# Optimization experiments

Measured on AMD Instinct MI355X. Metric: run time of the kernel, lower is better.

The kernel has to match this reference:

```python
import jax, jax.numpy as jnp
import numpy as np

N_NODES = 100000
N_EDGES = 3200000
F_IN = 128
CHANNELS = 128


def setup_inputs() -> dict:
    key = jax.random.key(0)
    k1, k2, k3, k4, k5 = jax.random.split(key, 5)
    x = jax.random.normal(k1, (N_NODES, F_IN), dtype=jnp.float32)
    kernel = jax.random.normal(k2, (F_IN, CHANNELS), dtype=jnp.float32) * (1.0 / np.sqrt(F_IN))
    bias = jnp.zeros((CHANNELS,), dtype=jnp.float32)
    edge_row = jnp.sort(jax.random.randint(k3, (N_EDGES,), 0, N_NODES, dtype=jnp.int32))
    edge_col = jax.random.randint(k4, (N_EDGES,), 0, N_NODES, dtype=jnp.int32)
    edge_val = jax.random.uniform(k5, (N_EDGES,), dtype=jnp.float32)
    return {"x": x, "kernel": kernel, "bias": bias, "edge_val": edge_val,
            "edge_row": edge_row, "edge_col": edge_col}


def reference(x, kernel, bias, edge_val, edge_row, edge_col):
    # Z = relu(A_tilde @ (X @ W) + b), A_tilde given in COO form (row, col, val)
    n = x.shape[0]
    xw = x @ kernel                              # [N, C] dense projection
    msgs = xw[edge_col] * edge_val[:, None]      # [E, C] gather + scale
    agg = jax.ops.segment_sum(msgs, edge_row, num_segments=n)  # SpMM scatter
    return jax.nn.relu(agg + bias)
```

## Files before the change

kernel.cpp:

```cpp
#include <hip/hip_runtime.h>

#define F_IN 128
#define CH   128

typedef __attribute__((ext_vector_type(8))) short bf16x8;
typedef __attribute__((ext_vector_type(4))) float f32x4;
typedef __attribute__((ext_vector_type(4))) unsigned u32x4;

static __device__ __forceinline__ ushort f2b(float f) {
  union { float f; unsigned u; } v; v.f = f;
  const unsigned u = v.u;
  return (ushort)((u + 0x7FFFu + ((u >> 16) & 1u)) >> 16);
}

__global__ __launch_bounds__(512) void gemm_rowptr_fused(
    const float* __restrict__ x, const float* __restrict__ w,
    unsigned char* __restrict__ xwq, float* __restrict__ scale,
    const int* __restrict__ edge_row, int* __restrict__ row_ptr,
    int n, int n_edges, int gemm_blocks) {
  __shared__ __align__(16) ushort Wt[F_IN * CH];
  const int t = threadIdx.x;

  if ((int)blockIdx.x >= gemm_blocks) {
    const int r = ((int)blockIdx.x - gemm_blocks) * 512 + t;
    if (r <= n) {
      int lo = 0, hi = n_edges;
      while (lo < hi) {
        const int mid = (lo + hi) >> 1;
        if (edge_row[mid] < r) lo = mid + 1; else hi = mid;
      }
      row_ptr[r] = lo;
    }
    return;
  }

  for (int i = t; i < (F_IN * CH) / 4; i += 512) {
    const int k  = i >> 5;
    const int n4 = (i & 31) << 2;
    const f32x4 wv = *(const f32x4*)&w[k * CH + n4];
#pragma unroll
    for (int q = 0; q < 4; ++q) {
      const int nn = n4 + q;
      const int byte = (nn * 256 + k * 2) ^ ((nn & 7) << 4);
      *(ushort*)((char*)Wt + byte) = f2b(wv[q]);
    }
  }
  __syncthreads();

  const int wave = t >> 6, lane = t & 63;
  const int R0   = blockIdx.x * 128 + wave * 16;
  const int arow = R0 + (lane & 15);
  const int kgrp = (lane >> 4) * 8;

  bf16x8 a[4];
#pragma unroll
  for (int s = 0; s < 4; ++s) {
    if (arow < n) {
      const f32x4 p0 = __builtin_nontemporal_load(
          (const f32x4*)&x[arow * F_IN + s * 32 + kgrp]);
      const f32x4 p1 = __builtin_nontemporal_load(
          (const f32x4*)&x[arow * F_IN + s * 32 + kgrp + 4]);
#pragma unroll
      for (int j = 0; j < 4; ++j) {
        a[s][j]     = (short)f2b(p0[j]);
        a[s][j + 4] = (short)f2b(p1[j]);
      }
    } else {
#pragma unroll
      for (int j = 0; j < 8; ++j) a[s][j] = (short)0;
    }
  }

  f32x4 acc[8];
#pragma unroll
  for (int t8 = 0; t8 < 8; ++t8) acc[t8] = (f32x4){0.f, 0.f, 0.f, 0.f};

#pragma unroll
  for (int t8 = 0; t8 < 8; ++t8) {
    const int col = t8 * 16 + (lane & 15);
#pragma unroll
    for (int s = 0; s < 4; ++s) {
      const int byte = (col * 256 + (s * 32 + kgrp) * 2) ^ ((col & 7) << 4);
      const bf16x8 b = *(const bf16x8*)((const char*)Wt + byte);
      acc[t8] = __builtin_amdgcn_mfma_f32_16x16x32_bf16(a[s], b, acc[t8], 0, 0, 0);
    }
  }

  const int li = lane & 15;
  const int r0 = R0 + (lane >> 4) * 4;
#pragma unroll
  for (int i = 0; i < 4; ++i) {
    const int rr = r0 + i;
    float m = 0.f;
#pragma unroll
    for (int t8 = 0; t8 < 8; ++t8) m = fmaxf(m, fabsf(acc[t8][i]));
    m = fmaxf(m, __shfl_xor(m, 1));
    m = fmaxf(m, __shfl_xor(m, 2));
    m = fmaxf(m, __shfl_xor(m, 4));
    m = fmaxf(m, __shfl_xor(m, 8));
    const float inv = (m > 1e-20f) ? 127.f / m : 0.f;
    if (rr < n) {
      if (li == 0) scale[rr] = m * (1.f / 127.f);
#pragma unroll
      for (int t8 = 0; t8 < 8; ++t8) {
        const float q = rintf(acc[t8][i] * inv) + 128.f;
        xwq[rr * CH + t8 * 16 + li] = (unsigned char)q;
      }
    }
  }
}

#define ACC16(U, V)                                                     \
  do {                                                                  \
    acc[ 0] = fmaf((V), (float)((U)[0]         & 0xFFu), acc[ 0]);      \
    acc[ 1] = fmaf((V), (float)(((U)[0] >>  8) & 0xFFu), acc[ 1]);      \
    acc[ 2] = fmaf((V), (float)(((U)[0] >> 16) & 0xFFu), acc[ 2]);      \
    acc[ 3] = fmaf((V), (float)((U)[0] >> 24),           acc[ 3]);      \
    acc[ 4] = fmaf((V), (float)((U)[1]         & 0xFFu), acc[ 4]);      \
    acc[ 5] = fmaf((V), (float)(((U)[1] >>  8) & 0xFFu), acc[ 5]);      \
    acc[ 6] = fmaf((V), (float)(((U)[1] >> 16) & 0xFFu), acc[ 6]);      \
    acc[ 7] = fmaf((V), (float)((U)[1] >> 24),           acc[ 7]);      \
    acc[ 8] = fmaf((V), (float)((U)[2]         & 0xFFu), acc[ 8]);      \
    acc[ 9] = fmaf((V), (float)(((U)[2] >>  8) & 0xFFu), acc[ 9]);      \
    acc[10] = fmaf((V), (float)(((U)[2] >> 16) & 0xFFu), acc[10]);      \
    acc[11] = fmaf((V), (float)((U)[2] >> 24),           acc[11]);      \
    acc[12] = fmaf((V), (float)((U)[3]         & 0xFFu), acc[12]);      \
    acc[13] = fmaf((V), (float)(((U)[3] >>  8) & 0xFFu), acc[13]);      \
    acc[14] = fmaf((V), (float)(((U)[3] >> 16) & 0xFFu), acc[14]);      \
    acc[15] = fmaf((V), (float)((U)[3] >> 24),           acc[15]);      \
  } while (0)

__global__ __launch_bounds__(256) void spmm_rowwave(
    const unsigned char* __restrict__ xwq, const float* __restrict__ scale,
    const float* __restrict__ edge_val, const int* __restrict__ edge_col,
    const int* __restrict__ row_ptr, const float* __restrict__ bias,
    float* __restrict__ out, int n) {
  const int wid = (int)((blockIdx.x * blockDim.x + threadIdx.x) >> 6);
  if (wid >= n) return;
  const int lane = threadIdx.x & 63;
  const int g8 = lane >> 3;
  const int l8 = lane & 7;
  const int start = row_ptr[wid], end = row_ptr[wid + 1];
  const u32x4* __restrict__ xw4 = (const u32x4*)xwq;

  float acc[16];
#pragma unroll
  for (int j = 0; j < 16; ++j) acc[j] = 0.f;
  float S = 0.f;

  for (int e0 = start; e0 < end; e0 += 64) {
    const int e = e0 + lane;
    int   c_my = 0;
    float vp_my = 0.f;
    if (e < end) {
      c_my = __builtin_nontemporal_load(edge_col + e);
      const float v = __builtin_nontemporal_load(edge_val + e);
      vp_my = v * scale[c_my];
    }
    S += vp_my;

#pragma unroll
    for (int it = 0; it < 8; ++it) {
      const int src  = it * 8 + g8;
      const int   c  = __shfl(c_my, src);
      const float vp = __shfl(vp_my, src);
      const u32x4 u = xw4[c * 8 + l8];
      ACC16(u, vp);
    }
  }

  S += __shfl_xor(S, 1);
  S += __shfl_xor(S, 2);
  S += __shfl_xor(S, 4);
  S += __shfl_xor(S, 8);
  S += __shfl_xor(S, 16);
  S += __shfl_xor(S, 32);

#pragma unroll
  for (int j = 0; j < 16; ++j) {
    acc[j] += __shfl_xor(acc[j], 8);
    acc[j] += __shfl_xor(acc[j], 16);
    acc[j] += __shfl_xor(acc[j], 32);
  }

  if (g8 == 0) {
    const int c = l8 * 16;
    const float off = 128.f * S;
#pragma unroll
    for (int q = 0; q < 4; ++q) {
      const f32x4 bv = *(const f32x4*)&bias[c + q * 4];
      f32x4 o;
      o[0] = fmaxf(acc[q * 4 + 0] - off + bv[0], 0.f);
      o[1] = fmaxf(acc[q * 4 + 1] - off + bv[1], 0.f);
      o[2] = fmaxf(acc[q * 4 + 2] - off + bv[2], 0.f);
      o[3] = fmaxf(acc[q * 4 + 3] - off + bv[3], 0.f);
      __builtin_nontemporal_store(o, (f32x4*)&out[(size_t)wid * CH + c + q * 4]);
    }
  }
}

extern "C" void kernel_launch(void* const* d_in, const int* in_sizes, int n_in,
                              void* d_out, int out_size, void* d_ws, size_t ws_size,
                              hipStream_t stream) {
  const float* x        = (const float*)d_in[0];
  const float* kernel   = (const float*)d_in[1];
  const float* bias     = (const float*)d_in[2];
  const float* edge_val = (const float*)d_in[3];
  const int*   edge_row = (const int*)d_in[4];
  const int*   edge_col = (const int*)d_in[5];
  float* out = (float*)d_out;

  const int n       = in_sizes[0] / F_IN;
  const int n_edges = in_sizes[3];

  unsigned char* xwq = (unsigned char*)d_ws;
  float* scale = (float*)((char*)d_ws + (size_t)n * CH);
  int* rowptr  = (int*)((char*)d_ws + (size_t)n * CH + (size_t)n * sizeof(float));

  const int GB = (n + 127) / 128;
  const int RB = (n + 1 + 511) / 512;
  gemm_rowptr_fused<<<GB + RB, 512, 0, stream>>>(x, kernel, xwq, scale,
                                                 edge_row, rowptr,
                                                 n, n_edges, GB);

  spmm_rowwave<<<(n + 3) / 4, 256, 0, stream>>>(xwq, scale, edge_val, edge_col,
                                                rowptr, bias, out, n);
}
```

Before: 132.1 us.

## Map sixteen lanes per row in SpMM with LDS-broadcast columns and packed FMA

The SpMM kernel moves from one 64-lane wave per row to sixteen lanes per row, each lane owning 8 output channels. Edge columns and scaled values are staged in shared memory, so each lane issues sixteen independent 8-byte gathers before accumulating with packed two-wide FMAs. This removes the cross-lane accumulator reduction and the idle lanes at the average degree of about 32, and adds memory-level parallelism. It relies on wave-synchronous LDS use without a barrier and uses more registers for the batched gathers.

```diff
diff --git a/kernel.cpp b/kernel.cpp
--- a/kernel.cpp
+++ b/kernel.cpp
@@ -5,7 +5,8 @@
 
 typedef __attribute__((ext_vector_type(8))) short bf16x8;
 typedef __attribute__((ext_vector_type(4))) float f32x4;
-typedef __attribute__((ext_vector_type(4))) unsigned u32x4;
+typedef __attribute__((ext_vector_type(2))) float f32x2;
+typedef __attribute__((ext_vector_type(2))) unsigned u32x2;
 
 static __device__ __forceinline__ ushort f2b(float f) {
   union { float f; unsigned u; } v; v.f = f;
@@ -110,62 +111,74 @@
   }
 }
 
-#define ACC16(U, V)                                                     \
-  do {                                                                  \
-    acc[ 0] = fmaf((V), (float)((U)[0]         & 0xFFu), acc[ 0]);      \
-    acc[ 1] = fmaf((V), (float)(((U)[0] >>  8) & 0xFFu), acc[ 1]);      \
-    acc[ 2] = fmaf((V), (float)(((U)[0] >> 16) & 0xFFu), acc[ 2]);      \
-    acc[ 3] = fmaf((V), (float)((U)[0] >> 24),           acc[ 3]);      \
-    acc[ 4] = fmaf((V), (float)((U)[1]         & 0xFFu), acc[ 4]);      \
-    acc[ 5] = fmaf((V), (float)(((U)[1] >>  8) & 0xFFu), acc[ 5]);      \
-    acc[ 6] = fmaf((V), (float)(((U)[1] >> 16) & 0xFFu), acc[ 6]);      \
-    acc[ 7] = fmaf((V), (float)((U)[1] >> 24),           acc[ 7]);      \
-    acc[ 8] = fmaf((V), (float)((U)[2]         & 0xFFu), acc[ 8]);      \
-    acc[ 9] = fmaf((V), (float)(((U)[2] >>  8) & 0xFFu), acc[ 9]);      \
-    acc[10] = fmaf((V), (float)(((U)[2] >> 16) & 0xFFu), acc[10]);      \
-    acc[11] = fmaf((V), (float)((U)[2] >> 24),           acc[11]);      \
-    acc[12] = fmaf((V), (float)((U)[3]         & 0xFFu), acc[12]);      \
-    acc[13] = fmaf((V), (float)(((U)[3] >>  8) & 0xFFu), acc[13]);      \
-    acc[14] = fmaf((V), (float)(((U)[3] >> 16) & 0xFFu), acc[14]);      \
-    acc[15] = fmaf((V), (float)((U)[3] >> 24),           acc[15]);      \
+#define ACCD(word, j0, vv)                                                \
+  do {                                                                    \
+    f32x2 lo_, hi_;                                                       \
+    lo_[0] = (float)((word) & 0xFFu);                                     \
+    lo_[1] = (float)(((word) >> 8) & 0xFFu);                              \
+    hi_[0] = (float)(((word) >> 16) & 0xFFu);                             \
+    hi_[1] = (float)((word) >> 24);                                       \
+    acc2[(j0)]     = __builtin_elementwise_fma(vv, lo_, acc2[(j0)]);      \
+    acc2[(j0) + 1] = __builtin_elementwise_fma(vv, hi_, acc2[(j0) + 1]);  \
   } while (0)
 
-__global__ __launch_bounds__(256) void spmm_rowwave(
+#define ACC8PK(U, V)                                                      \
+  do {                                                                    \
+    const f32x2 vv_ = {(V), (V)};                                         \
+    ACCD((U)[0], 0, vv_);                                                 \
+    ACCD((U)[1], 2, vv_);                                                 \
+  } while (0)
+
+__global__ __launch_bounds__(256) void spmm_qwave(
     const unsigned char* __restrict__ xwq, const float* __restrict__ scale,
     const float* __restrict__ edge_val, const int* __restrict__ edge_col,
     const int* __restrict__ row_ptr, const float* __restrict__ bias,
     float* __restrict__ out, int n) {
-  const int wid = (int)((blockIdx.x * blockDim.x + threadIdx.x) >> 6);
-  if (wid >= n) return;
-  const int lane = threadIdx.x & 63;
-  const int g8 = lane >> 3;
-  const int l8 = lane & 7;
-  const int start = row_ptr[wid], end = row_ptr[wid + 1];
-  const u32x4* __restrict__ xw4 = (const u32x4*)xwq;
-
-  float acc[16];
-#pragma unroll
-  for (int j = 0; j < 16; ++j) acc[j] = 0.f;
+  __shared__ int   cbuf[256];
+  __shared__ float vbuf[256];
+  const int tid = threadIdx.x;
+  const int row = (int)((blockIdx.x * 256 + tid) >> 4);
+  if (row >= n) return;
+  const int li    = tid & 15;
+  const int qbase = tid & ~15;
+  const u32x2* __restrict__ xw2 = (const u32x2*)xwq;
+
+  const int start = row_ptr[row], end = row_ptr[row + 1];
+
+  f32x2 acc2[4];
+#pragma unroll
+  for (int j = 0; j < 4; ++j) acc2[j] = (f32x2){0.f, 0.f};
   float S = 0.f;
 
-  for (int e0 = start; e0 < end; e0 += 64) {
-    const int e = e0 + lane;
+  for (int e0 = start; e0 < end; e0 += 16) {
+    const int e = e0 + li;
     int   c_my = 0;
     float vp_my = 0.f;
     if (e < end) {
       c_my = __builtin_nontemporal_load(edge_col + e);
-      const float v = __builtin_nontemporal_load(edge_val + e);
-      vp_my = v * scale[c_my];
+      vp_my = __builtin_nontemporal_load(edge_val + e) * scale[c_my];
     }
     S += vp_my;
-
-#pragma unroll
-    for (int it = 0; it < 8; ++it) {
-      const int src  = it * 8 + g8;
-      const int   c  = __shfl(c_my, src);
-      const float vp = __shfl(vp_my, src);
-      const u32x4 u = xw4[c * 8 + l8];
-      ACC16(u, vp);
+    cbuf[tid] = c_my;
+    vbuf[tid] = vp_my;
+
+    u32x2 u[16];
+#pragma unroll
+    for (int it4 = 0; it4 < 4; ++it4) {
+      const int4 c4 = *(const int4*)&cbuf[qbase + it4 * 4];
+      u[it4 * 4 + 0] = xw2[c4.x * 16 + li];
+      u[it4 * 4 + 1] = xw2[c4.y * 16 + li];
+      u[it4 * 4 + 2] = xw2[c4.z * 16 + li];
+      u[it4 * 4 + 3] = xw2[c4.w * 16 + li];
+    }
+
+#pragma unroll
+    for (int it4 = 0; it4 < 4; ++it4) {
+      const f32x4 v4 = *(const f32x4*)&vbuf[qbase + it4 * 4];
+      ACC8PK(u[it4 * 4 + 0], v4[0]);
+      ACC8PK(u[it4 * 4 + 1], v4[1]);
+      ACC8PK(u[it4 * 4 + 2], v4[2]);
+      ACC8PK(u[it4 * 4 + 3], v4[3]);
     }
   }
 
@@ -173,30 +186,23 @@
   S += __shfl_xor(S, 2);
   S += __shfl_xor(S, 4);
   S += __shfl_xor(S, 8);
-  S += __shfl_xor(S, 16);
-  S += __shfl_xor(S, 32);
-
-#pragma unroll
-  for (int j = 0; j < 16; ++j) {
-    acc[j] += __shfl_xor(acc[j], 8);
-    acc[j] += __shfl_xor(acc[j], 16);
-    acc[j] += __shfl_xor(acc[j], 32);
-  }
-
-  if (g8 == 0) {
-    const int c = l8 * 16;
-    const float off = 128.f * S;
-#pragma unroll
-    for (int q = 0; q < 4; ++q) {
-      const f32x4 bv = *(const f32x4*)&bias[c + q * 4];
-      f32x4 o;
-      o[0] = fmaxf(acc[q * 4 + 0] - off + bv[0], 0.f);
-      o[1] = fmaxf(acc[q * 4 + 1] - off + bv[1], 0.f);
-      o[2] = fmaxf(acc[q * 4 + 2] - off + bv[2], 0.f);
-      o[3] = fmaxf(acc[q * 4 + 3] - off + bv[3], 0.f);
-      __builtin_nontemporal_store(o, (f32x4*)&out[(size_t)wid * CH + c + q * 4]);
-    }
-  }
+
+  const float off = 128.f * S;
+  const float* a = (const float*)acc2;
+  const int cb = li * 8;
+  const f32x4 b0 = *(const f32x4*)&bias[cb];
+  const f32x4 b1 = *(const f32x4*)&bias[cb + 4];
+  f32x4 o0, o1;
+  o0[0] = fmaxf(a[0] - off + b0[0], 0.f);
+  o0[1] = fmaxf(a[1] - off + b0[1], 0.f);
+  o0[2] = fmaxf(a[2] - off + b0[2], 0.f);
+  o0[3] = fmaxf(a[3] - off + b0[3], 0.f);
+  o1[0] = fmaxf(a[4] - off + b1[0], 0.f);
+  o1[1] = fmaxf(a[5] - off + b1[1], 0.f);
+  o1[2] = fmaxf(a[6] - off + b1[2], 0.f);
+  o1[3] = fmaxf(a[7] - off + b1[3], 0.f);
+  __builtin_nontemporal_store(o0, (f32x4*)&out[(size_t)row * CH + cb]);
+  __builtin_nontemporal_store(o1, (f32x4*)&out[(size_t)row * CH + cb + 4]);
 }
 
 extern "C" void kernel_launch(void* const* d_in, const int* in_sizes, int n_in,
@@ -223,6 +229,7 @@
                                                  edge_row, rowptr,
                                                  n, n_edges, GB);
 
-  spmm_rowwave<<<(n + 3) / 4, 256, 0, stream>>>(xwq, scale, edge_val, edge_col,
-                                                rowptr, bias, out, n);
-}
+  const int blocks = (n * 16 + 255) / 256;
+  spmm_qwave<<<blocks, 256, 0, stream>>>(xwq, scale, edge_val, edge_col,
+                                         rowptr, bias, out, n);
+}
```

New measurement: 112.5 us. 1.17x faster.
